# Performance work log

Hardware: AMD Instinct MI355X
Metric: run time of the kernel (lower is better)

The kernel has to match this reference:

```python
import jax, jax.numpy as jnp
import numpy as np

N_ITEM = 100000
D = 512
CODEBOOK = 2048
B = 2048
K = 200
PAD = 0


def setup_inputs() -> dict:
    key = jax.random.key(0)
    ks = jax.random.split(key, 10)
    user_id = jax.random.randint(ks[0], (B,), 0, 100000)
    interacted_items = jax.random.randint(ks[1], (B, K), 0, N_ITEM + 1)
    pos = jax.random.randint(ks[2], (B,), 0, N_ITEM + 1)
    neg = jax.random.randint(ks[3], (B,), 0, N_ITEM + 1)
    item_embed = jax.random.normal(ks[4], (N_ITEM + 1, D), dtype=jnp.float32) * 0.01
    # map MLP: latent_dim -> 2*latent_dim -> latent_dim (PyTorch default init scale-ish)
    W1 = jax.random.normal(ks[5], (D, 2 * D), dtype=jnp.float32) * (1.0 / np.sqrt(D))
    b1 = jnp.zeros((2 * D,), dtype=jnp.float32)
    W2 = jax.random.normal(ks[6], (2 * D, D), dtype=jnp.float32) * (1.0 / np.sqrt(2 * D))
    b2 = jnp.zeros((D,), dtype=jnp.float32)
    codebook = jax.random.normal(ks[7], (CODEBOOK, D), dtype=jnp.float32)
    return {
        "user_id": user_id,
        "interacted_items": interacted_items,
        "pos": pos,
        "neg": neg,
        "item_embed": item_embed,
        "W1": W1,
        "b1": b1,
        "W2": W2,
        "b2": b2,
        "codebook": codebook,
    }


def reference(user_id, interacted_items, pos, neg, item_embed, W1, b1, W2, b2, codebook):
    # mask out padding, masked mean over history (user_embed_method == 'item')
    keep = (interacted_items != PAD).astype(item_embed.dtype)[..., None]  # [B,K,1]
    hist = item_embed[interacted_items]                                   # [B,K,D]
    mean_item = jnp.sum(hist * keep, axis=1) / jnp.sum(keep, axis=1)      # [B,D]
    # map MLP
    user_embed = jax.nn.relu(mean_item @ W1 + b1) @ W2 + b2               # [B,D]
    # VQ quantize (eval mode: no EMA update): squared-distance argmin dispatch
    d2 = (
        jnp.sum(user_embed * user_embed, axis=1, keepdims=True)
        - 2.0 * user_embed @ codebook.T
        + jnp.sum(codebook * codebook, axis=1)[None, :]
    )                                                                     # [B,CODEBOOK]
    id_t = jnp.argmin(d2, axis=1)                                         # [B]
    q = codebook[id_t]                                                    # [B,D]
    diff = jnp.mean((jax.lax.stop_gradient(q) - user_embed) ** 2)         # scalar commitment loss
    quant_user = user_embed + jax.lax.stop_gradient(q - user_embed)       # straight-through
    pos_item = item_embed[pos]                                            # [B,D]
    neg_item = item_embed[neg]                                            # [B,D]
    return (quant_user, pos_item, neg_item, diff, user_embed)
```

## Files before the change

### kernel.cpp

```cpp
#include <hip/hip_runtime.h>

typedef unsigned short u16;
typedef unsigned long long u64;
typedef __attribute__((ext_vector_type(8))) short short8;
typedef __attribute__((ext_vector_type(4))) float f32x4;

#define B_ 2048
#define D_ 512
#define CB_ 2048
#define K_ 200
#define NITEM_ 100001

__device__ __forceinline__ u16 f2bf_rne(float f) {
    unsigned u = __float_as_uint(f);
    unsigned r = (u + 0x7fffu + ((u >> 16) & 1u)) >> 16;
    return (u16)r;
}

__device__ __forceinline__ u64 shfl_xor_u64(u64 v, int m) {
    int lo = __shfl_xor((int)(v & 0xffffffffu), m);
    int hi = __shfl_xor((int)(v >> 32), m);
    return ((u64)(unsigned)hi << 32) | (unsigned)lo;
}

__global__ void cbprep_kernel(const float* __restrict__ cb, u16* __restrict__ ch,
                              float* __restrict__ cnormf, float* __restrict__ diffacc) {
    __shared__ double red[128];
    int j = blockIdx.x, t = threadIdx.x;
    float4 v = ((const float4*)(cb + (size_t)j * D_))[t];
    ushort4 o;
    o.x = f2bf_rne(v.x); o.y = f2bf_rne(v.y); o.z = f2bf_rne(v.z); o.w = f2bf_rne(v.w);
    ((ushort4*)(ch + (size_t)j * D_))[t] = o;
    red[t] = (double)v.x * v.x + (double)v.y * v.y + (double)v.z * v.z + (double)v.w * v.w;
    __syncthreads();
    for (int s = 64; s > 0; s >>= 1) {
        if (t < s) red[t] += red[t + s];
        __syncthreads();
    }
    if (t == 0) {
        cnormf[j] = (float)red[0];
        if (j == 0) diffacc[0] = 0.0f;
    }
}

__global__ void transpose_w(const float* __restrict__ W, u16* __restrict__ WT, int K, int N) {
    __shared__ float tile[32][33];
    int n0 = blockIdx.x * 32, k0 = blockIdx.y * 32;
    int t = threadIdx.x;
    int kl = t >> 3, nl = (t & 7) * 4;
    float4 v = *(const float4*)(W + (size_t)(k0 + kl) * N + n0 + nl);
    tile[kl][nl] = v.x; tile[kl][nl + 1] = v.y; tile[kl][nl + 2] = v.z; tile[kl][nl + 3] = v.w;
    __syncthreads();
    int nl2 = t >> 3, kl2 = (t & 7) * 4;
    ushort4 o;
    o.x = f2bf_rne(tile[kl2][nl2]);
    o.y = f2bf_rne(tile[kl2 + 1][nl2]);
    o.z = f2bf_rne(tile[kl2 + 2][nl2]);
    o.w = f2bf_rne(tile[kl2 + 3][nl2]);
    *(ushort4*)(WT + (size_t)(n0 + nl2) * K + k0 + kl2) = o;
}

__global__ void ie2q8_kernel(const float* __restrict__ ie, char* __restrict__ q8,
                             float* __restrict__ scales) {
    int gw = (blockIdx.x * 256 + threadIdx.x) >> 6;
    int lane = threadIdx.x & 63;
    int nw = (gridDim.x * 256) >> 6;
    for (int row = gw; row < NITEM_; row += nw) {
        const float* rp = ie + (size_t)row * D_ + lane * 8;
        float4 a = *(const float4*)rp;
        float4 b = *(const float4*)(rp + 4);
        float m = fmaxf(fmaxf(fmaxf(fabsf(a.x), fabsf(a.y)), fmaxf(fabsf(a.z), fabsf(a.w))),
                        fmaxf(fmaxf(fabsf(b.x), fabsf(b.y)), fmaxf(fabsf(b.z), fabsf(b.w))));
#pragma unroll
        for (int off = 32; off >= 1; off >>= 1)
            m = fmaxf(m, __shfl_xor(m, off));
        float inv = (m > 0.f) ? 127.0f / m : 0.f;
        float s = m * (1.0f / 127.0f);
        int q0 = __float2int_rn(a.x * inv) & 255;
        int q1 = __float2int_rn(a.y * inv) & 255;
        int q2 = __float2int_rn(a.z * inv) & 255;
        int q3 = __float2int_rn(a.w * inv) & 255;
        int q4 = __float2int_rn(b.x * inv) & 255;
        int q5 = __float2int_rn(b.y * inv) & 255;
        int q6 = __float2int_rn(b.z * inv) & 255;
        int q7 = __float2int_rn(b.w * inv) & 255;
        uint2 o;
        o.x = (unsigned)(q0 | (q1 << 8) | (q2 << 16) | (q3 << 24));
        o.y = (unsigned)(q4 | (q5 << 8) | (q6 << 16) | (q7 << 24));
        *(uint2*)(q8 + (size_t)row * D_ + lane * 8) = o;
        if (lane == 0) scales[row] = s;
    }
}

__global__ void mean_kernel_q8(const int* __restrict__ items,
                               const char* __restrict__ q8,
                               const float* __restrict__ scales,
                               u16* __restrict__ meanb) {
    __shared__ int sidx[K_];
    __shared__ float rs[3][64][8];
    __shared__ int rn_[4];
    int b = blockIdx.x, t = threadIdx.x;
    for (int k = t; k < K_; k += 256) sidx[k] = items[b * K_ + k];
    __syncthreads();
    int team = t >> 6;
    int lt = t & 63;
    float s[8] = {0.f, 0.f, 0.f, 0.f, 0.f, 0.f, 0.f, 0.f};
    int n0 = 0;
    int k0 = team * (K_ / 4);
#pragma unroll 4
    for (int k = k0; k < k0 + K_ / 4; k++) {
        int idx = sidx[k];
        n0 += (idx == 0) ? 1 : 0;
        float sc = scales[idx];
        uint2 qv = *(const uint2*)(q8 + (size_t)idx * D_ + lt * 8);
        unsigned dx = qv.x, dy = qv.y;
        s[0] += (float)((int)(dx << 24) >> 24) * sc;
        s[1] += (float)((int)(dx << 16) >> 24) * sc;
        s[2] += (float)((int)(dx <<  8) >> 24) * sc;
        s[3] += (float)((int)dx >> 24) * sc;
        s[4] += (float)((int)(dy << 24) >> 24) * sc;
        s[5] += (float)((int)(dy << 16) >> 24) * sc;
        s[6] += (float)((int)(dy <<  8) >> 24) * sc;
        s[7] += (float)((int)dy >> 24) * sc;
    }
    if (team > 0) {
#pragma unroll
        for (int e = 0; e < 8; e++) rs[team - 1][lt][e] = s[e];
    }
    if (lt == 0) rn_[team] = n0;
    __syncthreads();
    if (team == 0) {
#pragma unroll
        for (int tm = 0; tm < 3; tm++)
#pragma unroll
            for (int e = 0; e < 8; e++) s[e] += rs[tm][lt][e];
        int n0t = rn_[0] + rn_[1] + rn_[2] + rn_[3];
        float inv = 1.0f / (float)(K_ - n0t);
        float fn0 = (float)n0t;
        float s0 = scales[0];
        uint2 q0 = *(const uint2*)(q8 + lt * 8);
        unsigned dx = q0.x, dy = q0.y;
        float r0[8];
        r0[0] = (float)((int)(dx << 24) >> 24) * s0;
        r0[1] = (float)((int)(dx << 16) >> 24) * s0;
        r0[2] = (float)((int)(dx <<  8) >> 24) * s0;
        r0[3] = (float)((int)dx >> 24) * s0;
        r0[4] = (float)((int)(dy << 24) >> 24) * s0;
        r0[5] = (float)((int)(dy << 16) >> 24) * s0;
        r0[6] = (float)((int)(dy <<  8) >> 24) * s0;
        r0[7] = (float)((int)dy >> 24) * s0;
        short8 o;
#pragma unroll
        for (int e = 0; e < 8; e++)
            o[e] = (short)f2bf_rne((s[e] - fn0 * r0[e]) * inv);
        *(short8*)(meanb + (size_t)b * D_ + lt * 8) = o;
    }
}

__global__ void mean_kernel_f32(const int* __restrict__ items,
                                const float* __restrict__ item_embed,
                                u16* __restrict__ meanb) {
    __shared__ int sidx[K_];
    __shared__ float4 rs4[128];
    __shared__ int rc;
    int b = blockIdx.x, t = threadIdx.x;
    for (int k = t; k < K_; k += 256) sidx[k] = items[b * K_ + k];
    __syncthreads();
    int team = t >> 7;
    int lt = t & 127;
    int c = lt * 4;
    float s0 = 0.f, s1 = 0.f, s2 = 0.f, s3 = 0.f;
    int cnt = 0;
    int k0 = team * (K_ / 2);
#pragma unroll 4
    for (int k = k0; k < k0 + K_ / 2; k++) {
        int idx = sidx[k];
        float m = (idx != 0) ? 1.0f : 0.0f;
        cnt += (idx != 0) ? 1 : 0;
        float4 v = *(const float4*)(item_embed + (size_t)idx * D_ + c);
        s0 += v.x * m; s1 += v.y * m; s2 += v.z * m; s3 += v.w * m;
    }
    if (team == 1) {
        float4 p; p.x = s0; p.y = s1; p.z = s2; p.w = s3;
        rs4[lt] = p;
        if (lt == 0) rc = cnt;
    }
    __syncthreads();
    if (team == 0) {
        float4 p = rs4[lt];
        s0 += p.x; s1 += p.y; s2 += p.z; s3 += p.w;
        cnt += rc;
        float inv = 1.0f / (float)cnt;
        ushort4 o;
        o.x = f2bf_rne(s0 * inv); o.y = f2bf_rne(s1 * inv);
        o.z = f2bf_rne(s2 * inv); o.w = f2bf_rne(s3 * inv);
        *(ushort4*)(meanb + (size_t)b * D_ + c) = o;
    }
}

__global__ void gemm1_mfma(const u16* __restrict__ meanb, const u16* __restrict__ W1T,
                           const float* __restrict__ b1w, u16* __restrict__ hb) {
    int t = threadIdx.x;
    int wid = blockIdx.x * 4 + (t >> 6);
    int lane = t & 63;
    int mt = wid >> 5, nt = wid & 31;
    int m0 = mt * 16, n0 = nt * 32;
    int mr = lane & 15, quad = lane >> 4, kb = quad * 8;
    const u16* ap  = meanb + (size_t)(m0 + mr) * 512 + kb;
    const u16* bp0 = W1T + (size_t)(n0 + mr) * 512 + kb;
    const u16* bp1 = bp0 + 16 * 512;
    f32x4 acc0 = {0.f, 0.f, 0.f, 0.f}, acc1 = {0.f, 0.f, 0.f, 0.f};
#pragma unroll
    for (int ks = 0; ks < 16; ks++) {
        short8 a  = *(const short8*)(ap  + ks * 32);
        short8 b0 = *(const short8*)(bp0 + ks * 32);
        short8 b1 = *(const short8*)(bp1 + ks * 32);
        acc0 = __builtin_amdgcn_mfma_f32_16x16x32_bf16(a, b0, acc0, 0, 0, 0);
        acc1 = __builtin_amdgcn_mfma_f32_16x16x32_bf16(a, b1, acc1, 0, 0, 0);
    }
    float bias0 = b1w[n0 + mr], bias1 = b1w[n0 + 16 + mr];
#pragma unroll
    for (int r = 0; r < 4; r++) {
        int m = m0 + quad * 4 + r;
        float v0 = acc0[r] + bias0; v0 = v0 > 0.f ? v0 : 0.f;
        float v1 = acc1[r] + bias1; v1 = v1 > 0.f ? v1 : 0.f;
        hb[(size_t)m * 1024 + n0 + mr]      = f2bf_rne(v0);
        hb[(size_t)m * 1024 + n0 + 16 + mr] = f2bf_rne(v1);
    }
}

__global__ void gemm2_mfma(const u16* __restrict__ hb, const u16* __restrict__ W2T,
                           const float* __restrict__ b2w,
                           float* __restrict__ out_ue, u16* __restrict__ uh) {
    int t = threadIdx.x;
    int wid = blockIdx.x * 4 + (t >> 6);
    int lane = t & 63;
    int mt = wid >> 5, nt = wid & 31;
    int m0 = mt * 16, n0 = nt * 16;
    int mr = lane & 15, quad = lane >> 4, kb = quad * 8;
    const u16* ap = hb  + (size_t)(m0 + mr) * 1024 + kb;
    const u16* bp = W2T + (size_t)(n0 + mr) * 1024 + kb;
    f32x4 acc0 = {0.f, 0.f, 0.f, 0.f}, acc1 = {0.f, 0.f, 0.f, 0.f};
#pragma unroll
    for (int ks = 0; ks < 16; ks++) {
        short8 a0 = *(const short8*)(ap + ks * 32);
        short8 b0 = *(const short8*)(bp + ks * 32);
        short8 a1 = *(const short8*)(ap + 512 + ks * 32);
        short8 b1 = *(const short8*)(bp + 512 + ks * 32);
        acc0 = __builtin_amdgcn_mfma_f32_16x16x32_bf16(a0, b0, acc0, 0, 0, 0);
        acc1 = __builtin_amdgcn_mfma_f32_16x16x32_bf16(a1, b1, acc1, 0, 0, 0);
    }
    float bias = b2w[n0 + mr];
#pragma unroll
    for (int r = 0; r < 4; r++) {
        int m = m0 + quad * 4 + r;
        float v = acc0[r] + acc1[r] + bias;
        size_t o = (size_t)m * 512 + n0 + mr;
        out_ue[o] = v;
        uh[o] = f2bf_rne(v);
    }
}

__global__ void score_mfma(const u16* __restrict__ uh,
                           const u16* __restrict__ ch,
                           const float* __restrict__ cnormf,
                           u64* __restrict__ pminS) {
    __shared__ u64 red2[64];
    int t = threadIdx.x, lane = t & 63, w = t >> 6;
    int ustrip = blockIdx.x >> 3, jstrip = blockIdx.x & 7;
    int u0 = ustrip * 16;
    int j0 = jstrip * 256 + w * 64;
    int mr = lane & 15, quad = lane >> 4, kb = quad * 8;

    short8 af[16];
    const u16* ap = uh + (size_t)(u0 + mr) * 512 + kb;
#pragma unroll
    for (int ks = 0; ks < 16; ks++) af[ks] = *(const short8*)(ap + ks * 32);

    u64 best[4] = {~0ull, ~0ull, ~0ull, ~0ull};
    for (int jt = 0; jt < 4; jt++) {
        int jb = j0 + jt * 16;
        const u16* bp = ch + (size_t)(jb + mr) * 512 + kb;
        f32x4 acc = {0.f, 0.f, 0.f, 0.f};
#pragma unroll
        for (int ks = 0; ks < 16; ks++) {
            short8 bv = *(const short8*)(bp + ks * 32);
            acc = __builtin_amdgcn_mfma_f32_16x16x32_bf16(af[ks], bv, acc, 0, 0, 0);
        }
        int n = jb + mr;
        float cn = cnormf[n];
#pragma unroll
        for (int r = 0; r < 4; r++) {
            float d2 = cn - 2.0f * acc[r];
            u64 p = (((u64)__float_as_uint(d2)) << 32) | (unsigned)n;
            if (p < best[r]) best[r] = p;
        }
    }
#pragma unroll
    for (int off = 8; off >= 1; off >>= 1)
#pragma unroll
        for (int r = 0; r < 4; r++) {
            u64 o = shfl_xor_u64(best[r], off);
            if (o < best[r]) best[r] = o;
        }
    if (mr == 0) {
#pragma unroll
        for (int r = 0; r < 4; r++) red2[w * 16 + quad * 4 + r] = best[r];
    }
    __syncthreads();
    if (t < 16) {
        u64 m = red2[t];
#pragma unroll
        for (int ww = 1; ww < 4; ww++) {
            u64 v = red2[ww * 16 + t];
            if (v < m) m = v;
        }
        pminS[(size_t)(u0 + t) * 8 + jstrip] = m;
    }
}

__global__ void finalize_user(const u64* __restrict__ pminS,
                              const float* __restrict__ ub,
                              const float* __restrict__ cb,
                              float* __restrict__ out0,
                              float* __restrict__ diffacc) {
    __shared__ u64 sm64[8];
    __shared__ unsigned sbest;
    __shared__ float red[256];
    int b = blockIdx.x, t = threadIdx.x;
    if (t < 8) sm64[t] = pminS[(size_t)b * 8 + t];
    __syncthreads();
    if (t == 0) {
        u64 m = sm64[0];
#pragma unroll
        for (int i = 1; i < 8; i++) if (sm64[i] < m) m = sm64[i];
        sbest = (unsigned)(m & 0xffffffffu);
    }
    __syncthreads();
    unsigned bestj = sbest;
    int c = t * 2;
    float2 qv = ((const float2*)(cb + (size_t)bestj * 512))[t];
    float w0 = ub[(size_t)b * 512 + c];
    float w1 = ub[(size_t)b * 512 + c + 1];
    float2 o;
    o.x = w0 + (qv.x - w0);
    o.y = w1 + (qv.y - w1);
    ((float2*)(out0 + (size_t)b * 512))[t] = o;
    float d0 = qv.x - w0, d1 = qv.y - w1;
    red[t] = d0 * d0 + d1 * d1;
    __syncthreads();
    for (int s = 128; s > 0; s >>= 1) {
        if (t < s) red[t] += red[t + s];
        __syncthreads();
    }
    if (t == 0) atomicAdd(diffacc, red[0]);
}

__global__ void gather_pn(const int* __restrict__ pos, const int* __restrict__ neg,
                          const float* __restrict__ ie,
                          float* __restrict__ out1, float* __restrict__ out2) {
    int b = blockIdx.x, t = threadIdx.x;
    int p = pos[b], n = neg[b];
    ((float4*)(out1 + (size_t)b * 512))[t] = ((const float4*)(ie + (size_t)p * 512))[t];
    ((float4*)(out2 + (size_t)b * 512))[t] = ((const float4*)(ie + (size_t)n * 512))[t];
}

__global__ void diff_final(const float* __restrict__ diffacc, float* __restrict__ out3) {
    if (threadIdx.x == 0)
        out3[0] = diffacc[0] * (1.0f / ((float)B_ * (float)D_));
}

extern "C" void kernel_launch(void* const* d_in, const int* in_sizes, int n_in,
                              void* d_out, int out_size, void* d_ws, size_t ws_size,
                              hipStream_t stream) {
    const int* items = (const int*)d_in[1];
    const int* pos   = (const int*)d_in[2];
    const int* neg   = (const int*)d_in[3];
    const float* item_embed = (const float*)d_in[4];
    const float* W1 = (const float*)d_in[5];
    const float* b1 = (const float*)d_in[6];
    const float* W2 = (const float*)d_in[7];
    const float* b2 = (const float*)d_in[8];
    const float* cb = (const float*)d_in[9];

    float* out0 = (float*)d_out;
    float* out1 = out0 + (size_t)B_ * D_;
    float* out2 = out1 + (size_t)B_ * D_;
    float* out3 = out2 + (size_t)B_ * D_;
    float* out4 = out3 + 1;

    u16* hb = (u16*)out1;

    char* wsb = (char*)d_ws;
    u16* meanb = (u16*)wsb;
    u16* W1T   = (u16*)(wsb + 2097152);
    u16* W2T   = (u16*)(wsb + 3145728);
    u16* uh    = (u16*)(wsb + 4194304);
    u16* ch    = (u16*)(wsb + 6291456);
    u64* pminS = (u64*)(wsb + 8388608);
    float* cnormf  = (float*)(wsb + 8519680);
    float* diffacc = (float*)(wsb + 8527872);
    char*  iq8     = (char*)(wsb + 8650752);
    float* iscal   = (float*)(wsb + 8650752 + 51200512);
    const size_t WS_NEED_Q8 = 8650752ull + 51200512ull + 400004ull;
    const bool use_q8 = (ws_size >= WS_NEED_Q8);

    cbprep_kernel<<<dim3(CB_), dim3(128), 0, stream>>>(cb, ch, cnormf, diffacc);
    transpose_w<<<dim3(32, 16), dim3(256), 0, stream>>>(W1, W1T, 512, 1024);
    transpose_w<<<dim3(16, 32), dim3(256), 0, stream>>>(W2, W2T, 1024, 512);
    if (use_q8) {
        ie2q8_kernel<<<dim3(2048), dim3(256), 0, stream>>>(item_embed, iq8, iscal);
        mean_kernel_q8<<<dim3(B_), dim3(256), 0, stream>>>(items, iq8, iscal, meanb);
    } else {
        mean_kernel_f32<<<dim3(B_), dim3(256), 0, stream>>>(items, item_embed, meanb);
    }
    gemm1_mfma<<<dim3(1024), dim3(256), 0, stream>>>(meanb, W1T, b1, hb);
    gemm2_mfma<<<dim3(1024), dim3(256), 0, stream>>>(hb, W2T, b2, out4, uh);
    score_mfma<<<dim3(1024), dim3(256), 0, stream>>>(uh, ch, cnormf, pminS);
    finalize_user<<<dim3(B_), dim3(256), 0, stream>>>(pminS, out4, cb, out0, diffacc);
    gather_pn<<<dim3(B_), dim3(128), 0, stream>>>(pos, neg, item_embed, out1, out2);
    diff_final<<<dim3(1), dim3(64), 0, stream>>>(diffacc, out3);
}
```

Before: 477.4 us.

## Fuse prep kernels into one launch and fold diff finalization into finalize

Merges codebook prep, both weight transposes, the pos/neg gather and item-table int8 quantization into a single block-indexed kernel, so these independent jobs run in one launch and overlap. The separate diff_final launch is replaced by a last-block ticket counter inside finalize_user. The hidden buffer moves to workspace so the gather can run early without being overwritten. This cuts launch count and tail idle time, but adds a larger workspace requirement and heterogeneous blocks within one grid.

```diff
diff --git a/kernel.cpp b/kernel.cpp
--- a/kernel.cpp
+++ b/kernel.cpp
@@ -23,8 +23,94 @@
     return ((u64)(unsigned)hi << 32) | (unsigned)lo;
 }
 
+__global__ void prep_misc(const float* __restrict__ cb, u16* __restrict__ ch,
+                          float* __restrict__ cnormf, float* __restrict__ diffacc,
+                          unsigned* __restrict__ ticket,
+                          const float* __restrict__ W1, u16* __restrict__ W1T,
+                          const float* __restrict__ W2, u16* __restrict__ W2T,
+                          const int* __restrict__ pos, const int* __restrict__ neg,
+                          const float* __restrict__ ie,
+                          float* __restrict__ out1, float* __restrict__ out2,
+                          char* __restrict__ q8, float* __restrict__ scales) {
+    __shared__ double red[256];
+    __shared__ float tile[32][33];
+    int b = blockIdx.x, t = threadIdx.x;
+    if (b < 2048) {
+        int j = b;
+        float2 v = ((const float2*)(cb + (size_t)j * D_))[t];
+        ushort2 o;
+        o.x = f2bf_rne(v.x); o.y = f2bf_rne(v.y);
+        ((ushort2*)(ch + (size_t)j * D_))[t] = o;
+        red[t] = (double)v.x * v.x + (double)v.y * v.y;
+        __syncthreads();
+        for (int s = 128; s > 0; s >>= 1) {
+            if (t < s) red[t] += red[t + s];
+            __syncthreads();
+        }
+        if (t == 0) {
+            cnormf[j] = (float)red[0];
+            if (j == 0) { diffacc[0] = 0.0f; ticket[0] = 0u; }
+        }
+    } else if (b < 3072) {
+        const float* W; u16* WT; int K, N, bx, by;
+        if (b < 2560) { W = W1; WT = W1T; K = 512;  N = 1024; int i = b - 2048; bx = i & 31; by = i >> 5; }
+        else          { W = W2; WT = W2T; K = 1024; N = 512;  int i = b - 2560; bx = i & 15; by = i >> 4; }
+        int n0 = bx * 32, k0 = by * 32;
+        int kl = t >> 3, nl = (t & 7) * 4;
+        float4 v = *(const float4*)(W + (size_t)(k0 + kl) * N + n0 + nl);
+        tile[kl][nl] = v.x; tile[kl][nl + 1] = v.y; tile[kl][nl + 2] = v.z; tile[kl][nl + 3] = v.w;
+        __syncthreads();
+        int nl2 = t >> 3, kl2 = (t & 7) * 4;
+        ushort4 o;
+        o.x = f2bf_rne(tile[kl2][nl2]);
+        o.y = f2bf_rne(tile[kl2 + 1][nl2]);
+        o.z = f2bf_rne(tile[kl2 + 2][nl2]);
+        o.w = f2bf_rne(tile[kl2 + 3][nl2]);
+        *(ushort4*)(WT + (size_t)(n0 + nl2) * K + k0 + kl2) = o;
+    } else if (b < 5120) {
+        int bb = b - 3072;
+        if (t < 128) {
+            int p = pos[bb];
+            ((float4*)(out1 + (size_t)bb * D_))[t] = ((const float4*)(ie + (size_t)p * D_))[t];
+        } else {
+            int n = neg[bb];
+            int t2 = t - 128;
+            ((float4*)(out2 + (size_t)bb * D_))[t2] = ((const float4*)(ie + (size_t)n * D_))[t2];
+        }
+    } else {
+        int gw = (b - 5120) * 4 + (t >> 6);
+        int lane = t & 63;
+        for (int row = gw; row < NITEM_; row += 8192) {
+            const float* rp = ie + (size_t)row * D_ + lane * 8;
+            float4 a = *(const float4*)rp;
+            float4 bb4 = *(const float4*)(rp + 4);
+            float m = fmaxf(fmaxf(fmaxf(fabsf(a.x), fabsf(a.y)), fmaxf(fabsf(a.z), fabsf(a.w))),
+                            fmaxf(fmaxf(fabsf(bb4.x), fabsf(bb4.y)), fmaxf(fabsf(bb4.z), fabsf(bb4.w))));
+#pragma unroll
+            for (int off = 32; off >= 1; off >>= 1)
+                m = fmaxf(m, __shfl_xor(m, off));
+            float inv = (m > 0.f) ? 127.0f / m : 0.f;
+            float s = m * (1.0f / 127.0f);
+            int q0 = __float2int_rn(a.x * inv) & 255;
+            int q1 = __float2int_rn(a.y * inv) & 255;
+            int q2 = __float2int_rn(a.z * inv) & 255;
+            int q3 = __float2int_rn(a.w * inv) & 255;
+            int q4 = __float2int_rn(bb4.x * inv) & 255;
+            int q5 = __float2int_rn(bb4.y * inv) & 255;
+            int q6 = __float2int_rn(bb4.z * inv) & 255;
+            int q7 = __float2int_rn(bb4.w * inv) & 255;
+            uint2 o;
+            o.x = (unsigned)(q0 | (q1 << 8) | (q2 << 16) | (q3 << 24));
+            o.y = (unsigned)(q4 | (q5 << 8) | (q6 << 16) | (q7 << 24));
+            *(uint2*)(q8 + (size_t)row * D_ + lane * 8) = o;
+            if (lane == 0) scales[row] = s;
+        }
+    }
+}
+
 __global__ void cbprep_kernel(const float* __restrict__ cb, u16* __restrict__ ch,
-                              float* __restrict__ cnormf, float* __restrict__ diffacc) {
+                              float* __restrict__ cnormf, float* __restrict__ diffacc,
+                              unsigned* __restrict__ ticket) {
     __shared__ double red[128];
     int j = blockIdx.x, t = threadIdx.x;
     float4 v = ((const float4*)(cb + (size_t)j * D_))[t];
@@ -39,7 +125,7 @@
     }
     if (t == 0) {
         cnormf[j] = (float)red[0];
-        if (j == 0) diffacc[0] = 0.0f;
+        if (j == 0) { diffacc[0] = 0.0f; ticket[0] = 0u; }
     }
 }
 
@@ -60,35 +146,53 @@
     *(ushort4*)(WT + (size_t)(n0 + nl2) * K + k0 + kl2) = o;
 }
 
-__global__ void ie2q8_kernel(const float* __restrict__ ie, char* __restrict__ q8,
-                             float* __restrict__ scales) {
-    int gw = (blockIdx.x * 256 + threadIdx.x) >> 6;
-    int lane = threadIdx.x & 63;
-    int nw = (gridDim.x * 256) >> 6;
-    for (int row = gw; row < NITEM_; row += nw) {
-        const float* rp = ie + (size_t)row * D_ + lane * 8;
-        float4 a = *(const float4*)rp;
-        float4 b = *(const float4*)(rp + 4);
-        float m = fmaxf(fmaxf(fmaxf(fabsf(a.x), fabsf(a.y)), fmaxf(fabsf(a.z), fabsf(a.w))),
-                        fmaxf(fmaxf(fabsf(b.x), fabsf(b.y)), fmaxf(fabsf(b.z), fabsf(b.w))));
-#pragma unroll
-        for (int off = 32; off >= 1; off >>= 1)
-            m = fmaxf(m, __shfl_xor(m, off));
-        float inv = (m > 0.f) ? 127.0f / m : 0.f;
-        float s = m * (1.0f / 127.0f);
-        int q0 = __float2int_rn(a.x * inv) & 255;
-        int q1 = __float2int_rn(a.y * inv) & 255;
-        int q2 = __float2int_rn(a.z * inv) & 255;
-        int q3 = __float2int_rn(a.w * inv) & 255;
-        int q4 = __float2int_rn(b.x * inv) & 255;
-        int q5 = __float2int_rn(b.y * inv) & 255;
-        int q6 = __float2int_rn(b.z * inv) & 255;
-        int q7 = __float2int_rn(b.w * inv) & 255;
-        uint2 o;
-        o.x = (unsigned)(q0 | (q1 << 8) | (q2 << 16) | (q3 << 24));
-        o.y = (unsigned)(q4 | (q5 << 8) | (q6 << 16) | (q7 << 24));
-        *(uint2*)(q8 + (size_t)row * D_ + lane * 8) = o;
-        if (lane == 0) scales[row] = s;
+__global__ void gather_pn(const int* __restrict__ pos, const int* __restrict__ neg,
+                          const float* __restrict__ ie,
+                          float* __restrict__ out1, float* __restrict__ out2) {
+    int b = blockIdx.x, t = threadIdx.x;
+    int p = pos[b], n = neg[b];
+    ((float4*)(out1 + (size_t)b * 512))[t] = ((const float4*)(ie + (size_t)p * 512))[t];
+    ((float4*)(out2 + (size_t)b * 512))[t] = ((const float4*)(ie + (size_t)n * 512))[t];
+}
+
+__global__ void mean_kernel_f32(const int* __restrict__ items,
+                                const float* __restrict__ item_embed,
+                                u16* __restrict__ meanb) {
+    __shared__ int sidx[K_];
+    __shared__ float4 rs4[128];
+    __shared__ int rc;
+    int b = blockIdx.x, t = threadIdx.x;
+    for (int k = t; k < K_; k += 256) sidx[k] = items[b * K_ + k];
+    __syncthreads();
+    int team = t >> 7;
+    int lt = t & 127;
+    int c = lt * 4;
+    float s0 = 0.f, s1 = 0.f, s2 = 0.f, s3 = 0.f;
+    int cnt = 0;
+    int k0 = team * (K_ / 2);
+#pragma unroll 4
+    for (int k = k0; k < k0 + K_ / 2; k++) {
+        int idx = sidx[k];
+        float m = (idx != 0) ? 1.0f : 0.0f;
+        cnt += (idx != 0) ? 1 : 0;
+        float4 v = *(const float4*)(item_embed + (size_t)idx * D_ + c);
+        s0 += v.x * m; s1 += v.y * m; s2 += v.z * m; s3 += v.w * m;
+    }
+    if (team == 1) {
+        float4 p; p.x = s0; p.y = s1; p.z = s2; p.w = s3;
+        rs4[lt] = p;
+        if (lt == 0) rc = cnt;
+    }
+    __syncthreads();
+    if (team == 0) {
+        float4 p = rs4[lt];
+        s0 += p.x; s1 += p.y; s2 += p.z; s3 += p.w;
+        cnt += rc;
+        float inv = 1.0f / (float)cnt;
+        ushort4 o;
+        o.x = f2bf_rne(s0 * inv); o.y = f2bf_rne(s1 * inv);
+        o.z = f2bf_rne(s2 * inv); o.w = f2bf_rne(s3 * inv);
+        *(ushort4*)(meanb + (size_t)b * D_ + c) = o;
     }
 }
 
@@ -157,47 +261,6 @@
     }
 }
 
-__global__ void mean_kernel_f32(const int* __restrict__ items,
-                                const float* __restrict__ item_embed,
-                                u16* __restrict__ meanb) {
-    __shared__ int sidx[K_];
-    __shared__ float4 rs4[128];
-    __shared__ int rc;
-    int b = blockIdx.x, t = threadIdx.x;
-    for (int k = t; k < K_; k += 256) sidx[k] = items[b * K_ + k];
-    __syncthreads();
-    int team = t >> 7;
-    int lt = t & 127;
-    int c = lt * 4;
-    float s0 = 0.f, s1 = 0.f, s2 = 0.f, s3 = 0.f;
-    int cnt = 0;
-    int k0 = team * (K_ / 2);
-#pragma unroll 4
-    for (int k = k0; k < k0 + K_ / 2; k++) {
-        int idx = sidx[k];
-        float m = (idx != 0) ? 1.0f : 0.0f;
-        cnt += (idx != 0) ? 1 : 0;
-        float4 v = *(const float4*)(item_embed + (size_t)idx * D_ + c);
-        s0 += v.x * m; s1 += v.y * m; s2 += v.z * m; s3 += v.w * m;
-    }
-    if (team == 1) {
-        float4 p; p.x = s0; p.y = s1; p.z = s2; p.w = s3;
-        rs4[lt] = p;
-        if (lt == 0) rc = cnt;
-    }
-    __syncthreads();
-    if (team == 0) {
-        float4 p = rs4[lt];
-        s0 += p.x; s1 += p.y; s2 += p.z; s3 += p.w;
-        cnt += rc;
-        float inv = 1.0f / (float)cnt;
-        ushort4 o;
-        o.x = f2bf_rne(s0 * inv); o.y = f2bf_rne(s1 * inv);
-        o.z = f2bf_rne(s2 * inv); o.w = f2bf_rne(s3 * inv);
-        *(ushort4*)(meanb + (size_t)b * D_ + c) = o;
-    }
-}
-
 __global__ void gemm1_mfma(const u16* __restrict__ meanb, const u16* __restrict__ W1T,
                            const float* __restrict__ b1w, u16* __restrict__ hb) {
     int t = threadIdx.x;
@@ -323,7 +386,9 @@
                               const float* __restrict__ ub,
                               const float* __restrict__ cb,
                               float* __restrict__ out0,
-                              float* __restrict__ diffacc) {
+                              float* __restrict__ diffacc,
+                              unsigned* __restrict__ ticket,
+                              float* __restrict__ out3) {
     __shared__ u64 sm64[8];
     __shared__ unsigned sbest;
     __shared__ float red[256];
@@ -353,21 +418,16 @@
         if (t < s) red[t] += red[t + s];
         __syncthreads();
     }
-    if (t == 0) atomicAdd(diffacc, red[0]);
-}
-
-__global__ void gather_pn(const int* __restrict__ pos, const int* __restrict__ neg,
-                          const float* __restrict__ ie,
-                          float* __restrict__ out1, float* __restrict__ out2) {
-    int b = blockIdx.x, t = threadIdx.x;
-    int p = pos[b], n = neg[b];
-    ((float4*)(out1 + (size_t)b * 512))[t] = ((const float4*)(ie + (size_t)p * 512))[t];
-    ((float4*)(out2 + (size_t)b * 512))[t] = ((const float4*)(ie + (size_t)n * 512))[t];
-}
-
-__global__ void diff_final(const float* __restrict__ diffacc, float* __restrict__ out3) {
-    if (threadIdx.x == 0)
-        out3[0] = diffacc[0] * (1.0f / ((float)B_ * (float)D_));
+    if (t == 0) {
+        atomicAdd(diffacc, red[0]);
+        __threadfence();
+        unsigned my = atomicAdd(ticket, 1u);
+        if (my == (unsigned)(B_ - 1)) {
+            __threadfence();
+            float total = atomicAdd(diffacc, 0.0f);
+            out3[0] = total * (1.0f / ((float)B_ * (float)D_));
+        }
+    }
 }
 
 extern "C" void kernel_launch(void* const* d_in, const int* in_sizes, int n_in,
@@ -389,8 +449,6 @@
     float* out3 = out2 + (size_t)B_ * D_;
     float* out4 = out3 + 1;
 
-    u16* hb = (u16*)out1;
-
     char* wsb = (char*)d_ws;
     u16* meanb = (u16*)wsb;
     u16* W1T   = (u16*)(wsb + 2097152);
@@ -398,26 +456,34 @@
     u16* uh    = (u16*)(wsb + 4194304);
     u16* ch    = (u16*)(wsb + 6291456);
     u64* pminS = (u64*)(wsb + 8388608);
-    float* cnormf  = (float*)(wsb + 8519680);
-    float* diffacc = (float*)(wsb + 8527872);
-    char*  iq8     = (char*)(wsb + 8650752);
-    float* iscal   = (float*)(wsb + 8650752 + 51200512);
-    const size_t WS_NEED_Q8 = 8650752ull + 51200512ull + 400004ull;
-    const bool use_q8 = (ws_size >= WS_NEED_Q8);
-
-    cbprep_kernel<<<dim3(CB_), dim3(128), 0, stream>>>(cb, ch, cnormf, diffacc);
-    transpose_w<<<dim3(32, 16), dim3(256), 0, stream>>>(W1, W1T, 512, 1024);
-    transpose_w<<<dim3(16, 32), dim3(256), 0, stream>>>(W2, W2T, 1024, 512);
-    if (use_q8) {
-        ie2q8_kernel<<<dim3(2048), dim3(256), 0, stream>>>(item_embed, iq8, iscal);
+    float* cnormf   = (float*)(wsb + 8519680);
+    float* diffacc  = (float*)(wsb + 8527872);
+    unsigned* ticket = (unsigned*)(wsb + 8527876);
+    u16* hbw   = (u16*)(wsb + 8650752);
+    char*  iq8  = (char*)(wsb + 12845056);
+    float* iscal = (float*)(wsb + 64045568);
+    const size_t WS_NEED_FULL = 64445572ull;
+    const bool fused = (ws_size >= WS_NEED_FULL);
+
+    if (fused) {
+        prep_misc<<<dim3(7168), dim3(256), 0, stream>>>(
+            cb, ch, cnormf, diffacc, ticket, W1, W1T, W2, W2T,
+            pos, neg, item_embed, out1, out2, iq8, iscal);
         mean_kernel_q8<<<dim3(B_), dim3(256), 0, stream>>>(items, iq8, iscal, meanb);
+        gemm1_mfma<<<dim3(1024), dim3(256), 0, stream>>>(meanb, W1T, b1, hbw);
+        gemm2_mfma<<<dim3(1024), dim3(256), 0, stream>>>(hbw, W2T, b2, out4, uh);
+        score_mfma<<<dim3(1024), dim3(256), 0, stream>>>(uh, ch, cnormf, pminS);
+        finalize_user<<<dim3(B_), dim3(256), 0, stream>>>(pminS, out4, cb, out0, diffacc, ticket, out3);
     } else {
+        u16* hb = (u16*)out1;
+        cbprep_kernel<<<dim3(CB_), dim3(128), 0, stream>>>(cb, ch, cnormf, diffacc, ticket);
+        transpose_w<<<dim3(32, 16), dim3(256), 0, stream>>>(W1, W1T, 512, 1024);
+        transpose_w<<<dim3(16, 32), dim3(256), 0, stream>>>(W2, W2T, 1024, 512);
         mean_kernel_f32<<<dim3(B_), dim3(256), 0, stream>>>(items, item_embed, meanb);
-    }
-    gemm1_mfma<<<dim3(1024), dim3(256), 0, stream>>>(meanb, W1T, b1, hb);
-    gemm2_mfma<<<dim3(1024), dim3(256), 0, stream>>>(hb, W2T, b2, out4, uh);
-    score_mfma<<<dim3(1024), dim3(256), 0, stream>>>(uh, ch, cnormf, pminS);
-    finalize_user<<<dim3(B_), dim3(256), 0, stream>>>(pminS, out4, cb, out0, diffacc);
-    gather_pn<<<dim3(B_), dim3(128), 0, stream>>>(pos, neg, item_embed, out1, out2);
-    diff_final<<<dim3(1), dim3(64), 0, stream>>>(diffacc, out3);
-}
+        gemm1_mfma<<<dim3(1024), dim3(256), 0, stream>>>(meanb, W1T, b1, hb);
+        gemm2_mfma<<<dim3(1024), dim3(256), 0, stream>>>(hb, W2T, b2, out4, uh);
+        score_mfma<<<dim3(1024), dim3(256), 0, stream>>>(uh, ch, cnormf, pminS);
+        finalize_user<<<dim3(B_), dim3(256), 0, stream>>>(pminS, out4, cb, out0, diffacc, ticket, out3);
+        gather_pn<<<dim3(B_), dim3(128), 0, stream>>>(pos, neg, item_embed, out1, out2);
+    }
+}
```

New measurement: 497.0 us. 1.04x slower.
